# Kernel tuning notes

Measured on AMD Instinct MI355X. Metric: run time of the kernel, lower is better.

The kernel has to match this reference:

```python
import jax, jax.numpy as jnp
import numpy as np

B, S, D = 2, 2048, 768
H = 12
HD = D // H  # 64
SCALE = HD ** -0.5


def setup_inputs() -> dict:
    key = jax.random.key(0)
    k1, k2, k3, k4, k5 = jax.random.split(key, 5)
    x = jax.random.normal(k1, (B, S, D), dtype=jnp.float32)
    w_qkv = jax.random.normal(k2, (D, 3 * D), dtype=jnp.float32) * (D ** -0.5)
    b_qkv = jax.random.normal(k3, (3 * D,), dtype=jnp.float32) * 0.02
    w_proj = jax.random.normal(k4, (D, D), dtype=jnp.float32) * (D ** -0.5)
    b_proj = jax.random.normal(k5, (D,), dtype=jnp.float32) * 0.02
    return {"x": x, "w_qkv": w_qkv, "b_qkv": b_qkv, "w_proj": w_proj, "b_proj": b_proj}


def reference(x, w_qkv, b_qkv, w_proj, b_proj):
    b, s, d = x.shape
    # QKV projection: (B,S,3D) -> (3,B,H,S,HD)
    qkv = x @ w_qkv + b_qkv
    qkv = qkv.reshape(b, s, 3, H, HD).transpose(2, 0, 3, 1, 4)
    q, k, v = qkv[0], qkv[1], qkv[2]
    q = q * SCALE
    # full NxN attention scores, as in the original module
    attn = jnp.einsum("bhqd,bhkd->bhqk", q, k)
    attn = jax.nn.softmax(attn, axis=-1)
    out = jnp.einsum("bhqk,bhkd->bhqd", attn, v)  # (B,H,S,HD)
    out = out.transpose(0, 2, 1, 3).reshape(b, s, d)
    return out @ w_proj + b_proj
```

## Files before the change

### kernel.cpp

```cpp
#include <hip/hip_runtime.h>
#include <hip/hip_bf16.h>

#define B_ 2
#define S_ 2048
#define D_ 768
#define H_ 12
#define HD_ 64
#define EXP2C_ 0.1803368801111244f

typedef __attribute__((ext_vector_type(8))) short bf16x8;
typedef __attribute__((ext_vector_type(8))) unsigned short u16x8;
typedef __attribute__((ext_vector_type(4))) float f32x4;
typedef __attribute__((ext_vector_type(4))) unsigned int u32x4;

static __device__ __forceinline__ unsigned short f2bf(float x) {
    union { float f; unsigned u; } v; v.f = x;
    unsigned r = (v.u + 0x7FFFu + ((v.u >> 16) & 1u)) >> 16;
    return (unsigned short)r;
}
static __device__ __forceinline__ float bf2f(unsigned short h) {
    union { unsigned u; float f; } v; v.u = ((unsigned)h) << 16;
    return v.f;
}
static __device__ __forceinline__ float fexp2(float x) { return __builtin_exp2f(x); }

static __device__ __forceinline__ unsigned pk_bf16(float a, float b) {
    __hip_bfloat162 pk = __float22bfloat162_rn(make_float2(a, b));
    union { __hip_bfloat162 h; unsigned u; } v; v.h = pk;
    return v.u;
}

static __device__ __forceinline__ f32x4 mfma32(bf16x8 a, bf16x8 b, f32x4 c) {
    return __builtin_amdgcn_mfma_f32_16x16x32_bf16(a, b, c, 0, 0, 0);
}

typedef __attribute__((address_space(3))) unsigned int lds_u32;
typedef __attribute__((address_space(1))) const unsigned int glb_u32;
static __device__ __forceinline__ void glds16(const unsigned short* g, unsigned short* l) {
    __builtin_amdgcn_global_load_lds((glb_u32*)g, (lds_u32*)l, 16, 0, 0);
}

#define PREP_CONV_ 1536
#define PREP_TQKV_ 1728
#define PREP_TPRJ_ 576
__global__ __launch_bounds__(256) void prep_kernel(
    const float* __restrict__ x,      unsigned short* __restrict__ x16,
    const float* __restrict__ w_qkv,  unsigned short* __restrict__ wqkvT,
    const float* __restrict__ w_proj, unsigned short* __restrict__ wprojT)
{
    __shared__ float tile[32][33];
    const int bid = blockIdx.x, t = threadIdx.x;
    if (bid < PREP_CONV_) {
        const int i = (bid * 256 + t) * 8;
        float4 a0 = *(const float4*)(x + i);
        float4 a1 = *(const float4*)(x + i + 4);
        u16x8 s;
        s[0] = f2bf(a0.x); s[1] = f2bf(a0.y); s[2] = f2bf(a0.z); s[3] = f2bf(a0.w);
        s[4] = f2bf(a1.x); s[5] = f2bf(a1.y); s[6] = f2bf(a1.z); s[7] = f2bf(a1.w);
        *(u16x8*)(x16 + i) = s;
        return;
    }
    const float* w; unsigned short* wT; int N, bb;
    if (bid < PREP_CONV_ + PREP_TQKV_) { w = w_qkv; wT = wqkvT; N = 3 * D_; bb = bid - PREP_CONV_; }
    else                               { w = w_proj; wT = wprojT; N = D_;   bb = bid - PREP_CONV_ - PREP_TQKV_; }
    const int K = D_;
    const int nt = N / 32;
    const int n0 = (bb % nt) * 32, k0 = (bb / nt) * 32;
    const int tx = t & 31, ty = t >> 5;
#pragma unroll
    for (int i = 0; i < 4; i++)
        tile[ty + i * 8][tx] = w[(size_t)(k0 + ty + i * 8) * N + n0 + tx];
    __syncthreads();
#pragma unroll
    for (int i = 0; i < 4; i++)
        wT[(size_t)(n0 + ty + i * 8) * K + k0 + tx] = f2bf(tile[tx][ty + i * 8]);
}

template <int BM, int BN, bool OUT_F32, bool VSPLIT>
__global__ __launch_bounds__(256) void gemm_bt_kernel(
    const unsigned short* __restrict__ A,
    const unsigned short* __restrict__ Bt,
    const float* __restrict__ bias,
    void* __restrict__ Cp,
    unsigned short* __restrict__ vt,
    int M, int N, int K)
{
    constexpr int BK = 64;
    __shared__ __align__(16) unsigned short As[BM][BK];
    __shared__ __align__(16) unsigned short Bs[BN][BK];
    constexpr int MI = BM / 32, NJ = BN / 32;
    constexpr int ACH = BM * BK / 8;
    constexpr int BCH = BN * BK / 8;

    const int t = threadIdx.x;
    const int w = t >> 6, lane = t & 63, quad = lane >> 4, l16 = lane & 15;
    const int n0 = blockIdx.x * BN, m0 = blockIdx.y * BM;
    const int mw = (w & 1) * (BM / 2), nw = (w >> 1) * (BN / 2);

    const f32x4 z = {0.f, 0.f, 0.f, 0.f};
    f32x4 acc[MI][NJ];
#pragma unroll
    for (int i = 0; i < MI; i++)
#pragma unroll
        for (int j = 0; j < NJ; j++) acc[i][j] = z;

    for (int kk = 0; kk < K; kk += BK) {
#pragma unroll
        for (int it = 0; it < ACH / 256; it++) {
            const int c = t + it * 256;
            const int row = c >> 3, gs = (c & 7) ^ (row & 7);
            glds16(A + (size_t)(m0 + row) * K + kk + gs * 8, &As[0][0] + c * 8);
        }
#pragma unroll
        for (int it = 0; it < BCH / 256; it++) {
            const int c = t + it * 256;
            const int row = c >> 3, gs = (c & 7) ^ (row & 7);
            glds16(Bt + (size_t)(n0 + row) * K + kk + gs * 8, &Bs[0][0] + c * 8);
        }
        __syncthreads();

#pragma unroll
        for (int k2 = 0; k2 < 2; k2++) {
            bf16x8 a[MI], b[NJ];
#pragma unroll
            for (int i = 0; i < MI; i++) {
                const int row = mw + i * 16 + l16;
                const int p = (quad + k2 * 4) ^ (row & 7);
                a[i] = *(const bf16x8*)(&As[row][p * 8]);
            }
#pragma unroll
            for (int j = 0; j < NJ; j++) {
                const int row = nw + j * 16 + l16;
                const int p = (quad + k2 * 4) ^ (row & 7);
                b[j] = *(const bf16x8*)(&Bs[row][p * 8]);
            }
#pragma unroll
            for (int i = 0; i < MI; i++)
#pragma unroll
                for (int j = 0; j < NJ; j++)
                    acc[i][j] = mfma32(a[i], b[j], acc[i][j]);
        }
        __syncthreads();
    }

    if (VSPLIT && n0 >= 2 * D_) {
#pragma unroll
        for (int j = 0; j < NJ; j++) {
            const int gcol = n0 + nw + j * 16 + l16;
            const int col = gcol - 2 * D_;
            const int hh = col >> 6, hd = col & 63;
            const float bv = bias[gcol];
#pragma unroll
            for (int i = 0; i < MI; i++) {
                const int row = m0 + mw + i * 16 + quad * 4;
                const int bb = row >> 11, ss = row & 2047;
                unsigned long long pkv = 0;
#pragma unroll
                for (int r = 0; r < 4; r++)
                    pkv |= (unsigned long long)f2bf(acc[i][j][r] + bv) << (16 * r);
                *(unsigned long long*)(vt +
                    ((size_t)(bb * H_ + hh) * HD_ + hd) * S_ + ss) = pkv;
            }
        }
        return;
    }

#pragma unroll
    for (int j = 0; j < NJ; j++) {
        const int col = n0 + nw + j * 16 + l16;
        const float bv = bias[col];
#pragma unroll
        for (int i = 0; i < MI; i++) {
#pragma unroll
            for (int r = 0; r < 4; r++) {
                const int row = m0 + mw + i * 16 + quad * 4 + r;
                const float v = acc[i][j][r] + bv;
                if (OUT_F32) ((float*)Cp)[(size_t)row * N + col] = v;
                else         ((unsigned short*)Cp)[(size_t)row * N + col] = f2bf(v);
            }
        }
    }
}

__global__ __launch_bounds__(256) void attn_kernel(
    const unsigned short* __restrict__ qkv,
    const unsigned short* __restrict__ vt,
    float* __restrict__ o_p0,
    float* __restrict__ o_p1,
    float* __restrict__ l_p)
{
    __shared__ __align__(16) unsigned short Ks[2][64][64];
    __shared__ __align__(16) unsigned short Vs[2][64][64];

    const int t = threadIdx.x;
    const int w = t >> 6, lane = t & 63, quad = lane >> 4, l16 = lane & 15;
    const int h8 = l16 & 7;
    const int id = blockIdx.x;
    const int xcd = id & 7, ix = id >> 3;
    const int grp = xcd * 6 + (ix >> 5);
    const int qt = ix & 31;
    const int bh = grp >> 1, ks = grp & 1;
    const int b = bh / H_, h = bh % H_;
    const int ld = 3 * D_;

    const unsigned short* qbase =
        qkv + (size_t)(b * S_ + qt * 64 + 16 * w + l16) * ld + h * HD_;
    u16x8 qr0 = *(const u16x8*)(qbase + quad * 8);
    u16x8 qr1 = *(const u16x8*)(qbase + 32 + quad * 8);
    bf16x8 qf0, qf1;
#pragma unroll
    for (int j = 0; j < 8; j++) {
        qf0[j] = (short)f2bf(bf2f(qr0[j]) * EXP2C_);
        qf1[j] = (short)f2bf(bf2f(qr1[j]) * EXP2C_);
    }

    bf16x8 ones;
#pragma unroll
    for (int j = 0; j < 8; j++) ones[j] = (short)0x3F80;

    const unsigned short* kbase =
        qkv + (size_t)(b * S_ + ks * 1024) * ld + D_ + h * HD_;
    const unsigned short* vbase = vt + (size_t)bh * HD_ * S_;

    const int c0 = t, c1 = t + 256;
    const int row0 = c0 >> 3, row1 = c1 >> 3;
    const int kg0 = (c0 & 7) ^ ((row0 & 3) | (((row0 >> 3) & 1) << 2));
    const int kg1 = (c1 & 7) ^ ((row1 & 3) | (((row1 >> 3) & 1) << 2));
    const int vg0 = (c0 & 7) ^ (row0 & 7);
    const int vg1 = (c1 & 7) ^ (row1 & 7);
    const unsigned short* kp0 = kbase + (size_t)row0 * ld + kg0 * 8;
    const unsigned short* kp1 = kbase + (size_t)row1 * ld + kg1 * 8;
    const unsigned short* vp0 = vbase + (size_t)row0 * S_ + ks * 1024 + vg0 * 8;
    const unsigned short* vp1 = vbase + (size_t)row1 * S_ + ks * 1024 + vg1 * 8;
    const size_t KSTEP = (size_t)64 * ld;

    const f32x4 z = {0.f, 0.f, 0.f, 0.f};
    f32x4 o_acc[4] = {z, z, z, z};
    f32x4 l_acc = z;

    glds16(kp0, &Ks[0][0][0] + c0 * 8);
    glds16(kp1, &Ks[0][0][0] + c1 * 8);
    glds16(vp0, &Vs[0][0][0] + c0 * 8);
    glds16(vp1, &Vs[0][0][0] + c1 * 8);
    kp0 += KSTEP; kp1 += KSTEP; vp0 += 64; vp1 += 64;
    __syncthreads();

    const int NT = 1024 / 64;
    for (int kt = 0; kt < NT; kt++) {
        const int buf = kt & 1;

        if (kt + 1 < NT) {
            unsigned short* kd = &Ks[buf ^ 1][0][0];
            unsigned short* vd = &Vs[buf ^ 1][0][0];
            glds16(kp0, kd + c0 * 8);
            glds16(kp1, kd + c1 * 8);
            glds16(vp0, vd + c0 * 8);
            glds16(vp1, vd + c1 * 8);
            kp0 += KSTEP; kp1 += KSTEP; vp0 += 64; vp1 += 64;
        }

        f32x4 s_acc[4] = {z, z, z, z};
#pragma unroll
        for (int nt = 0; nt < 4; nt++) {
            const int rowp = ((nt >> 1) << 5) + ((l16 >> 2) << 3) + ((nt & 1) << 2) + (l16 & 3);
            const int skr = (rowp & 3) | (((rowp >> 3) & 1) << 2);
            const unsigned short* kr = &Ks[buf][rowp][0];
            bf16x8 k0 = *(const bf16x8*)(kr + (quad ^ skr) * 8);
            bf16x8 k1 = *(const bf16x8*)(kr + ((quad ^ skr) ^ 4) * 8);
            s_acc[nt] = mfma32(k0, qf0, s_acc[nt]);
            s_acc[nt] = mfma32(k1, qf1, s_acc[nt]);
        }

        bf16x8 vr0[4], vr1[4];
#pragma unroll
        for (int nt = 0; nt < 4; nt++) {
            const int row = nt * 16 + l16;
            vr0[nt] = *(const bf16x8*)(&Vs[buf][row][(quad ^ h8) * 8]);
            vr1[nt] = *(const bf16x8*)(&Vs[buf][row][((quad ^ h8) ^ 4) * 8]);
        }

        f32x4 pr[4];
#pragma unroll
        for (int nt = 0; nt < 4; nt++) {
#pragma unroll
            for (int r = 0; r < 4; r++) pr[nt][r] = fexp2(s_acc[nt][r]);
        }
        union { u32x4 u; bf16x8 h; } ca, cb;
        ca.u[0] = pk_bf16(pr[0][0], pr[0][1]);
        ca.u[1] = pk_bf16(pr[0][2], pr[0][3]);
        ca.u[2] = pk_bf16(pr[1][0], pr[1][1]);
        ca.u[3] = pk_bf16(pr[1][2], pr[1][3]);
        cb.u[0] = pk_bf16(pr[2][0], pr[2][1]);
        cb.u[1] = pk_bf16(pr[2][2], pr[2][3]);
        cb.u[2] = pk_bf16(pr[3][0], pr[3][1]);
        cb.u[3] = pk_bf16(pr[3][2], pr[3][3]);
        const bf16x8 pa0 = ca.h, pa1 = cb.h;

        l_acc = mfma32(pa0, ones, l_acc);
        l_acc = mfma32(pa1, ones, l_acc);

#pragma unroll
        for (int nt = 0; nt < 4; nt++) {
            o_acc[nt] = mfma32(pa0, vr0[nt], o_acc[nt]);
            o_acc[nt] = mfma32(pa1, vr1[nt], o_acc[nt]);
        }

        __syncthreads();
    }

    float* op = ks ? o_p1 : o_p0;
    float* lp2 = l_p + (size_t)ks * (B_ * S_ * H_);
#pragma unroll
    for (int r = 0; r < 4; r++) {
        const int row = b * S_ + qt * 64 + 16 * w + quad * 4 + r;
        float* ob = op + (size_t)row * D_ + h * HD_;
#pragma unroll
        for (int nt = 0; nt < 4; nt++)
            ob[nt * 16 + l16] = o_acc[nt][r];
        if (l16 == 0) lp2[(size_t)row * H_ + h] = l_acc[r];
    }
}

__global__ __launch_bounds__(256) void combine_kernel(
    const float* __restrict__ o_p0,
    const float* __restrict__ o_p1,
    const float* __restrict__ l_p,
    unsigned short* __restrict__ o)
{
    const int i = (blockIdx.x * 256 + threadIdx.x) * 8;
    const int row = i / D_, col = i - row * D_, h = col >> 6;
    const float l0 = l_p[(size_t)row * H_ + h];
    const float l1 = l_p[(size_t)(B_ * S_ * H_) + row * H_ + h];
    const float inv = 1.f / (l0 + l1);
    float4 a0 = *(const float4*)(o_p0 + i);
    float4 a1 = *(const float4*)(o_p0 + i + 4);
    float4 b0 = *(const float4*)(o_p1 + i);
    float4 b1 = *(const float4*)(o_p1 + i + 4);
    u16x8 s;
    s[0] = f2bf((a0.x + b0.x) * inv); s[1] = f2bf((a0.y + b0.y) * inv);
    s[2] = f2bf((a0.z + b0.z) * inv); s[3] = f2bf((a0.w + b0.w) * inv);
    s[4] = f2bf((a1.x + b1.x) * inv); s[5] = f2bf((a1.y + b1.y) * inv);
    s[6] = f2bf((a1.z + b1.z) * inv); s[7] = f2bf((a1.w + b1.w) * inv);
    *(u16x8*)(o + i) = s;
}

extern "C" void kernel_launch(void* const* d_in, const int* in_sizes, int n_in,
                              void* d_out, int out_size, void* d_ws, size_t ws_size,
                              hipStream_t stream) {
    const float* x      = (const float*)d_in[0];
    const float* w_qkv  = (const float*)d_in[1];
    const float* b_qkv  = (const float*)d_in[2];
    const float* w_proj = (const float*)d_in[3];
    const float* b_proj = (const float*)d_in[4];
    float* out = (float*)d_out;

    unsigned short* qkv    = (unsigned short*)d_ws;
    unsigned short* vtb    = qkv    + (size_t)(B_ * S_) * (3 * D_);
    unsigned short* o_x16  = vtb    + (size_t)(B_ * H_) * HD_ * S_;
    unsigned short* wqkvT  = o_x16  + (size_t)(B_ * S_) * D_;
    unsigned short* wprojT = wqkvT  + (size_t)D_ * (3 * D_);
    float* o_p1 = (float*)(wprojT + (size_t)D_ * D_);
    float* l_p  = o_p1 + (size_t)(B_ * S_) * D_;
    float* o_p0 = out;

    dim3 blk(256);
    prep_kernel<<<dim3(PREP_CONV_ + PREP_TQKV_ + PREP_TPRJ_), blk, 0, stream>>>(
        x, o_x16, w_qkv, wqkvT, w_proj, wprojT);
    gemm_bt_kernel<128, 96, false, true><<<dim3((3 * D_) / 96, (B_ * S_) / 128), blk, 0, stream>>>(
        o_x16, wqkvT, b_qkv, qkv, vtb, B_ * S_, 3 * D_, D_);
    attn_kernel<<<dim3((S_ / 64) * (B_ * H_) * 2), blk, 0, stream>>>(
        qkv, vtb, o_p0, o_p1, l_p);
    combine_kernel<<<dim3((B_ * S_) * D_ / (256 * 8)), blk, 0, stream>>>(
        o_p0, o_p1, l_p, o_x16);
    gemm_bt_kernel<64, 64, true, false><<<dim3(D_ / 64, (B_ * S_) / 64), blk, 0, stream>>>(
        o_x16, wprojT, b_proj, out, nullptr, B_ * S_, D_, D_);
}
```

Baseline: 165.5 us.

## Remove split-K attention and fuse normalization into attention epilogue

Attention blocks now process all 2048 keys instead of splitting keys across two blocks, and each block normalizes by its row sum and writes bf16 output directly. This eliminates the combine kernel and the fp32 partial output and row-sum buffers, cutting a launch and substantial memory traffic. In exchange the grid halves, reducing parallelism and latency hiding in the attention phase.

```diff
diff --git a/kernel.cpp b/kernel.cpp
--- a/kernel.cpp
+++ b/kernel.cpp
@@ -185,9 +185,7 @@
 __global__ __launch_bounds__(256) void attn_kernel(
     const unsigned short* __restrict__ qkv,
     const unsigned short* __restrict__ vt,
-    float* __restrict__ o_p0,
-    float* __restrict__ o_p1,
-    float* __restrict__ l_p)
+    unsigned short* __restrict__ o)
 {
     __shared__ __align__(16) unsigned short Ks[2][64][64];
     __shared__ __align__(16) unsigned short Vs[2][64][64];
@@ -197,9 +195,8 @@
     const int h8 = l16 & 7;
     const int id = blockIdx.x;
     const int xcd = id & 7, ix = id >> 3;
-    const int grp = xcd * 6 + (ix >> 5);
+    const int bh = xcd * 3 + (ix >> 5);
     const int qt = ix & 31;
-    const int bh = grp >> 1, ks = grp & 1;
     const int b = bh / H_, h = bh % H_;
     const int ld = 3 * D_;
 
@@ -218,8 +215,7 @@
 #pragma unroll
     for (int j = 0; j < 8; j++) ones[j] = (short)0x3F80;
 
-    const unsigned short* kbase =
-        qkv + (size_t)(b * S_ + ks * 1024) * ld + D_ + h * HD_;
+    const unsigned short* kbase = qkv + (size_t)(b * S_) * ld + D_ + h * HD_;
     const unsigned short* vbase = vt + (size_t)bh * HD_ * S_;
 
     const int c0 = t, c1 = t + 256;
@@ -230,8 +226,8 @@
     const int vg1 = (c1 & 7) ^ (row1 & 7);
     const unsigned short* kp0 = kbase + (size_t)row0 * ld + kg0 * 8;
     const unsigned short* kp1 = kbase + (size_t)row1 * ld + kg1 * 8;
-    const unsigned short* vp0 = vbase + (size_t)row0 * S_ + ks * 1024 + vg0 * 8;
-    const unsigned short* vp1 = vbase + (size_t)row1 * S_ + ks * 1024 + vg1 * 8;
+    const unsigned short* vp0 = vbase + (size_t)row0 * S_ + vg0 * 8;
+    const unsigned short* vp1 = vbase + (size_t)row1 * S_ + vg1 * 8;
     const size_t KSTEP = (size_t)64 * ld;
 
     const f32x4 z = {0.f, 0.f, 0.f, 0.f};
@@ -245,7 +241,7 @@
     kp0 += KSTEP; kp1 += KSTEP; vp0 += 64; vp1 += 64;
     __syncthreads();
 
-    const int NT = 1024 / 64;
+    const int NT = S_ / 64;
     for (int kt = 0; kt < NT; kt++) {
         const int buf = kt & 1;
 
@@ -308,40 +304,15 @@
         __syncthreads();
     }
 
-    float* op = ks ? o_p1 : o_p0;
-    float* lp2 = l_p + (size_t)ks * (B_ * S_ * H_);
 #pragma unroll
     for (int r = 0; r < 4; r++) {
+        const float inv = 1.f / l_acc[r];
         const int row = b * S_ + qt * 64 + 16 * w + quad * 4 + r;
-        float* ob = op + (size_t)row * D_ + h * HD_;
+        unsigned short* ob = o + (size_t)row * D_ + h * HD_;
 #pragma unroll
         for (int nt = 0; nt < 4; nt++)
-            ob[nt * 16 + l16] = o_acc[nt][r];
-        if (l16 == 0) lp2[(size_t)row * H_ + h] = l_acc[r];
-    }
-}
-
-__global__ __launch_bounds__(256) void combine_kernel(
-    const float* __restrict__ o_p0,
-    const float* __restrict__ o_p1,
-    const float* __restrict__ l_p,
-    unsigned short* __restrict__ o)
-{
-    const int i = (blockIdx.x * 256 + threadIdx.x) * 8;
-    const int row = i / D_, col = i - row * D_, h = col >> 6;
-    const float l0 = l_p[(size_t)row * H_ + h];
-    const float l1 = l_p[(size_t)(B_ * S_ * H_) + row * H_ + h];
-    const float inv = 1.f / (l0 + l1);
-    float4 a0 = *(const float4*)(o_p0 + i);
-    float4 a1 = *(const float4*)(o_p0 + i + 4);
-    float4 b0 = *(const float4*)(o_p1 + i);
-    float4 b1 = *(const float4*)(o_p1 + i + 4);
-    u16x8 s;
-    s[0] = f2bf((a0.x + b0.x) * inv); s[1] = f2bf((a0.y + b0.y) * inv);
-    s[2] = f2bf((a0.z + b0.z) * inv); s[3] = f2bf((a0.w + b0.w) * inv);
-    s[4] = f2bf((a1.x + b1.x) * inv); s[5] = f2bf((a1.y + b1.y) * inv);
-    s[6] = f2bf((a1.z + b1.z) * inv); s[7] = f2bf((a1.w + b1.w) * inv);
-    *(u16x8*)(o + i) = s;
+            ob[nt * 16 + l16] = f2bf(o_acc[nt][r] * inv);
+    }
 }
 
 extern "C" void kernel_launch(void* const* d_in, const int* in_sizes, int n_in,
@@ -359,19 +330,13 @@
     unsigned short* o_x16  = vtb    + (size_t)(B_ * H_) * HD_ * S_;
     unsigned short* wqkvT  = o_x16  + (size_t)(B_ * S_) * D_;
     unsigned short* wprojT = wqkvT  + (size_t)D_ * (3 * D_);
-    float* o_p1 = (float*)(wprojT + (size_t)D_ * D_);
-    float* l_p  = o_p1 + (size_t)(B_ * S_) * D_;
-    float* o_p0 = out;
 
     dim3 blk(256);
     prep_kernel<<<dim3(PREP_CONV_ + PREP_TQKV_ + PREP_TPRJ_), blk, 0, stream>>>(
         x, o_x16, w_qkv, wqkvT, w_proj, wprojT);
     gemm_bt_kernel<128, 96, false, true><<<dim3((3 * D_) / 96, (B_ * S_) / 128), blk, 0, stream>>>(
         o_x16, wqkvT, b_qkv, qkv, vtb, B_ * S_, 3 * D_, D_);
-    attn_kernel<<<dim3((S_ / 64) * (B_ * H_) * 2), blk, 0, stream>>>(
-        qkv, vtb, o_p0, o_p1, l_p);
-    combine_kernel<<<dim3((B_ * S_) * D_ / (256 * 8)), blk, 0, stream>>>(
-        o_p0, o_p1, l_p, o_x16);
+    attn_kernel<<<dim3((S_ / 64) * (B_ * H_)), blk, 0, stream>>>(qkv, vtb, o_x16);
     gemm_bt_kernel<64, 64, true, false><<<dim3(D_ / 64, (B_ * S_) / 64), blk, 0, stream>>>(
         o_x16, wprojT, b_proj, out, nullptr, B_ * S_, D_, D_);
 }
```

Result: no change. 163.1 us (-1.4%).
